# Kernel tuning notes

Hardware: AMD Instinct MI355X
Metric: run time of the kernel (lower is better)

The kernel has to match this reference:

```python
import math
import jax, jax.numpy as jnp
import numpy as np

B, T, C, H = 2, 2048, 1024, 16
D = C // H


def get_slopes(n):
    def pow2_slopes(n):
        start = 2.0 ** (-(2.0 ** (-(math.log2(n) - 3))))
        return [start * (start ** i) for i in range(n)]
    if math.log2(n).is_integer():
        return pow2_slopes(n)
    c = 2 ** math.floor(math.log2(n))
    return pow2_slopes(c) + get_slopes(2 * c)[0::2][: n - c]


def setup_inputs() -> dict:
    key = jax.random.key(0)
    ks = jax.random.split(key, 5)
    std = 0.02
    x = jax.random.normal(ks[0], (B, T, C), dtype=jnp.float32)
    Wq = std * jax.random.normal(ks[1], (C, C), dtype=jnp.float32)
    Wk = std * jax.random.normal(ks[2], (C, C), dtype=jnp.float32)
    Wv = std * jax.random.normal(ks[3], (C, C), dtype=jnp.float32)
    Wo = (std / math.sqrt(24)) * jax.random.normal(ks[4], (C, C), dtype=jnp.float32)
    z = jnp.zeros((C,), dtype=jnp.float32)
    return {"x": x, "Wq": Wq, "bq": z, "Wk": Wk, "bk": z, "Wv": Wv, "bv": z, "Wo": Wo, "bo": z}


def reference(x, Wq, bq, Wk, bk, Wv, bv, Wo, bo):
    b, t, c = x.shape
    h, d = H, c // H
    # qkv projections: nn.Linear computes x @ W.T + b
    q = (x @ Wq.T + bq).reshape(b, t, h, d).transpose(0, 2, 1, 3)  # [B,H,T,D]
    k = (x @ Wk.T + bk).reshape(b, t, h, d).transpose(0, 2, 1, 3)
    v = (x @ Wv.T + bv).reshape(b, t, h, d).transpose(0, 2, 1, 3)

    att = jnp.einsum("bhqd,bhkd->bhqk", q, k) * (1.0 / math.sqrt(d))

    # ALiBi bias: -slope_h * (i - j) on the lower triangle, 0 above
    slopes = jnp.asarray(get_slopes(h), dtype=x.dtype)  # [H]
    i = jnp.arange(t)
    rel = jnp.tril(i[:, None] - i[None, :]).astype(x.dtype)  # [T,T]
    alibi = -slopes[:, None, None] * rel  # [H,T,T]
    att = att + alibi[None, :, :, :]

    causal = jnp.tril(jnp.ones((t, t), dtype=bool))
    att = jnp.where(causal[None, None, :, :], att, -jnp.inf)
    att = jax.nn.softmax(att, axis=-1)

    y = jnp.einsum("bhqk,bhkd->bhqd", att, v)
    y = y.transpose(0, 2, 1, 3).reshape(b, t, c)
    return y @ Wo.T + bo
```

## Files before the change

### kernel.cpp

```cpp
#include <hip/hip_runtime.h>
#include <hip/hip_bf16.h>
#include <cstdint>
#include <cstddef>

#define B_ 2
#define T_ 2048
#define C_ 1024
#define H_ 16
#define D_ 64
#define BT_ (B_*T_)
#define QKV_S 3072

typedef __bf16 bf16;
typedef __bf16 bf16x4 __attribute__((ext_vector_type(4)));
typedef __bf16 bf16x8 __attribute__((ext_vector_type(8)));
typedef float f32x4 __attribute__((ext_vector_type(4)));

__global__ __launch_bounds__(256) void cast_all(const float* __restrict__ x,
                                                const float* __restrict__ wq,
                                                const float* __restrict__ wk,
                                                const float* __restrict__ wv,
                                                const float* __restrict__ wo,
                                                const float* __restrict__ bq,
                                                const float* __restrict__ bk,
                                                const float* __restrict__ bv,
                                                bf16* __restrict__ xb,
                                                bf16* __restrict__ wqkvb,
                                                bf16* __restrict__ wob,
                                                float* __restrict__ bqkv) {
  const int X4 = (BT_ * C_) / 4;
  const int W4 = (C_ * C_) / 4;
  int i = blockIdx.x * blockDim.x + threadIdx.x;
  if (i >= X4 + 4 * W4 + 768) return;
  if (i >= X4 + 4 * W4) {
    int idx = i - (X4 + 4 * W4);
    int w = idx >> 8, off = idx & 255;
    const float* src = (w == 0) ? bq : (w == 1) ? bk : bv;
    reinterpret_cast<float4*>(bqkv + w * C_)[off] = reinterpret_cast<const float4*>(src)[off];
    return;
  }
  const float* src;
  bf16* dst;
  int off;
  if (i < X4) {
    src = x; dst = xb; off = i;
  } else {
    int k = i - X4;
    int w = k >> 18;
    off = k & (W4 - 1);
    src = (w == 0) ? wq : (w == 1) ? wk : (w == 2) ? wv : wo;
    dst = (w < 3) ? (wqkvb + (size_t)w * C_ * C_) : wob;
  }
  float4 v = reinterpret_cast<const float4*>(src)[off];
  bf16x4 o;
  o[0] = (bf16)v.x; o[1] = (bf16)v.y; o[2] = (bf16)v.z; o[3] = (bf16)v.w;
  *reinterpret_cast<bf16x4*>(dst + (size_t)off * 4) = o;
}

template<typename OutT, bool FUSE_VT>
__global__ __launch_bounds__(256) void gemm_bt(const bf16* __restrict__ A,
                                               const bf16* __restrict__ Bm,
                                               const float* __restrict__ bias,
                                               OutT* __restrict__ Cout,
                                               bf16* __restrict__ VtOut,
                                               int M, int N, int K) {
  __shared__ bf16 As[3][128 * 32];
  __shared__ bf16 Bs[3][128 * 32];
  const int tid = threadIdx.x;
  const int wid = tid >> 6, lane = tid & 63;
  const int grp = lane >> 4, li = lane & 15;
  const int wr = wid >> 1, wc = wid & 1;
  const int m0 = blockIdx.y * 128, n0 = blockIdx.x * 128;

  f32x4 acc[4][4] = {};

  const int srow = lane >> 2;
  const int scol = (lane & 3) * 8;

  auto stage = [&](int k0, int bufi) __attribute__((always_inline)) {
#pragma unroll
    for (int p = 0; p < 2; ++p) {
      const int rbase = (p * 4 + wid) * 16;
      const bf16* ga = A + (size_t)(m0 + rbase + srow) * K + (k0 + scol);
      const bf16* gb = Bm + (size_t)(n0 + rbase + srow) * K + (k0 + scol);
      __builtin_amdgcn_global_load_lds((__attribute__((address_space(1))) void*)ga,
                                       (__attribute__((address_space(3))) void*)(&As[bufi][(p * 4 + wid) * 512]), 16, 0, 0);
      __builtin_amdgcn_global_load_lds((__attribute__((address_space(1))) void*)gb,
                                       (__attribute__((address_space(3))) void*)(&Bs[bufi][(p * 4 + wid) * 512]), 16, 0, 0);
    }
  };

  const int nt = K >> 5;
  stage(0, 0);
  if (nt > 1) stage(32, 1);
  int r = 0;
  for (int t = 0; t < nt; ++t) {
    if (t + 1 < nt) asm volatile("s_waitcnt vmcnt(4)\ns_barrier" ::: "memory");
    else            asm volatile("s_waitcnt vmcnt(0)\ns_barrier" ::: "memory");
    if (t + 2 < nt) stage((t + 2) * 32, (r == 0) ? 2 : r - 1);

    bf16x8 af[4], bfr[4];
#pragma unroll
    for (int m = 0; m < 4; ++m)
      af[m] = *reinterpret_cast<const bf16x8*>(&As[r][(wr * 64 + m * 16 + li) * 32 + grp * 8]);
#pragma unroll
    for (int n = 0; n < 4; ++n)
      bfr[n] = *reinterpret_cast<const bf16x8*>(&Bs[r][(wc * 64 + n * 16 + li) * 32 + grp * 8]);
#pragma unroll
    for (int m = 0; m < 4; ++m)
#pragma unroll
      for (int n = 0; n < 4; ++n)
        acc[m][n] = __builtin_amdgcn_mfma_f32_16x16x32_bf16(af[m], bfr[n], acc[m][n], 0, 0, 0);

    r = (r == 2) ? 0 : r + 1;
  }

  float bcol[4];
#pragma unroll
  for (int n = 0; n < 4; ++n) bcol[n] = bias[n0 + wc * 64 + n * 16 + li];

  if (FUSE_VT && n0 >= 2 * C_) {
#pragma unroll
    for (int m = 0; m < 4; ++m) {
      const int row0 = m0 + wr * 64 + m * 16 + grp * 4;
      const int b = row0 >> 11, t = row0 & (T_ - 1);
#pragma unroll
      for (int n = 0; n < 4; ++n) {
        const int hd = (n0 - 2 * C_) + wc * 64 + n * 16 + li;
        bf16x4 o4;
#pragma unroll
        for (int j = 0; j < 4; ++j) o4[j] = (bf16)(acc[m][n][j] + bcol[n]);
        *reinterpret_cast<bf16x4*>(VtOut + ((size_t)(b * C_ + hd)) * T_ + t) = o4;
      }
    }
  } else {
#pragma unroll
    for (int m = 0; m < 4; ++m) {
#pragma unroll
      for (int n = 0; n < 4; ++n) {
        const int col = n0 + wc * 64 + n * 16 + li;
#pragma unroll
        for (int j = 0; j < 4; ++j) {
          const int row = m0 + wr * 64 + m * 16 + grp * 4 + j;
          float v = acc[m][n][j] + bcol[n];
          Cout[(size_t)row * N + col] = (OutT)v;
        }
      }
    }
  }
}

__global__ __launch_bounds__(512) void attn_kernel(const bf16* __restrict__ qkv,
                                                   const bf16* __restrict__ Vt,
                                                   bf16* __restrict__ Y) {
  __shared__ bf16 Ks[4][64 * 64];
  __shared__ bf16 Vs[4][64 * 64];
  __shared__ bf16 Ps[8 * 16 * 72];

  const int tid = threadIdx.x;
  const int wid = tid >> 6, lane = tid & 63;
  const int grp = lane >> 4, li = lane & 15;
  const int bh = blockIdx.y;
  const int b = bh >> 4, h = bh & 15;
  const float slope = exp2f(-0.5f * (float)(h + 1));

  bf16* Pw = Ps + wid * (16 * 72);

  const bf16* Kbase = qkv + (size_t)b * T_ * QKV_S + C_ + (size_t)h * D_;
  const bf16* Vbase = Vt + (size_t)bh * D_ * T_;

  const int strow = tid >> 3;
  const int stswz = ((tid & 7) * 16) ^ ((strow & 7) << 4);
  const int rsw = (li & 7) << 4;

  auto stage = [&](int kv0, int bufi) __attribute__((always_inline)) {
    const bf16* gk = Kbase + (size_t)(kv0 + strow) * QKV_S + (stswz >> 1);
    const bf16* gv = Vbase + (size_t)strow * T_ + kv0 + (stswz >> 1);
    __builtin_amdgcn_global_load_lds((__attribute__((address_space(1))) void*)gk,
                                     (__attribute__((address_space(3))) void*)(&Ks[bufi][wid * 512]), 16, 0, 0);
    __builtin_amdgcn_global_load_lds((__attribute__((address_space(1))) void*)gv,
                                     (__attribute__((address_space(3))) void*)(&Vs[bufi][wid * 512]), 16, 0, 0);
  };

  auto do_qtile = [&](int QT) __attribute__((always_inline)) {
    const int q0 = QT * 128;
    const int wq0 = q0 + wid * 16;
    const int qi = wq0 + li;

    bf16x8 qf[2];
    {
      const bf16* qrow = qkv + (size_t)(b * T_ + qi) * QKV_S + h * D_;
      qf[0] = *reinterpret_cast<const bf16x8*>(qrow + grp * 8);
      qf[1] = *reinterpret_cast<const bf16x8*>(qrow + 32 + grp * 8);
#pragma unroll
      for (int c = 0; c < 2; ++c)
#pragma unroll
        for (int j = 0; j < 8; ++j)
          qf[c][j] = (bf16)((float)qf[c][j] * 0.125f);
    }

    f32x4 oacc[4] = {};
    float mrun = -1e30f, lrun = 0.f;

    auto compute = [&](int kv0, int bufi, bool masked) __attribute__((always_inline)) {
      const char* Kb = (const char*)&Ks[bufi][0];
      const char* Vb = (const char*)&Vs[bufi][0];

      f32x4 s[4] = {};
      __builtin_amdgcn_s_setprio(1);
#pragma unroll
      for (int n = 0; n < 4; ++n) {
        const char* kr = Kb + (n * 16 + li) * 128;
        bf16x8 kf0 = *reinterpret_cast<const bf16x8*>(kr + ((grp * 16) ^ rsw));
        bf16x8 kf1 = *reinterpret_cast<const bf16x8*>(kr + ((64 + grp * 16) ^ rsw));
        s[n] = __builtin_amdgcn_mfma_f32_16x16x32_bf16(kf0, qf[0], s[n], 0, 0, 0);
        s[n] = __builtin_amdgcn_mfma_f32_16x16x32_bf16(kf1, qf[1], s[n], 0, 0, 0);
      }
      __builtin_amdgcn_s_setprio(0);

      bf16x8 vr[2][4];
#pragma unroll
      for (int kc = 0; kc < 2; ++kc)
#pragma unroll
        for (int nd = 0; nd < 4; ++nd) {
          const char* vrp = Vb + (nd * 16 + li) * 128;
          vr[kc][nd] = *reinterpret_cast<const bf16x8*>(vrp + ((kc * 64 + grp * 16) ^ rsw));
        }

      float p[4][4];
      float rm = -1e30f;
#pragma unroll
      for (int n = 0; n < 4; ++n)
#pragma unroll
        for (int j = 0; j < 4; ++j) {
          const int kv = kv0 + n * 16 + grp * 4 + j;
          float sv = fmaf(-slope, (float)(qi - kv), s[n][j]);
          if (masked) sv = (kv <= qi) ? sv : -1e30f;
          p[n][j] = sv;
          rm = fmaxf(rm, sv);
        }
      rm = fmaxf(rm, __shfl_xor(rm, 16, 64));
      rm = fmaxf(rm, __shfl_xor(rm, 32, 64));
      if (!__all(rm - mrun <= 8.0f)) {
        const float mnew = fmaxf(mrun, rm);
        const float alpha = __expf(mrun - mnew);
        mrun = mnew;
        lrun *= alpha;
#pragma unroll
        for (int nd = 0; nd < 4; ++nd)
#pragma unroll
          for (int j = 0; j < 4; ++j)
            oacc[nd][j] *= alpha;
      }
      float rs = 0.f;
#pragma unroll
      for (int n = 0; n < 4; ++n)
#pragma unroll
        for (int j = 0; j < 4; ++j) {
          float e = __expf(p[n][j] - mrun);
          p[n][j] = e;
          rs += e;
        }
      rs += __shfl_xor(rs, 16, 64);
      rs += __shfl_xor(rs, 32, 64);
      lrun += rs;

#pragma unroll
      for (int n = 0; n < 4; ++n) {
        bf16x4 p4;
#pragma unroll
        for (int j = 0; j < 4; ++j) p4[j] = (bf16)p[n][j];
        *reinterpret_cast<bf16x4*>(Pw + li * 72 + n * 16 + grp * 4) = p4;
      }
      asm volatile("s_waitcnt lgkmcnt(0)" ::: "memory");
      __builtin_amdgcn_sched_barrier(0);

      __builtin_amdgcn_s_setprio(1);
#pragma unroll
      for (int kc = 0; kc < 2; ++kc) {
        bf16x8 pb = *reinterpret_cast<const bf16x8*>(Pw + li * 72 + kc * 32 + grp * 8);
#pragma unroll
        for (int nd = 0; nd < 4; ++nd)
          oacc[nd] = __builtin_amdgcn_mfma_f32_16x16x32_bf16(vr[kc][nd], pb, oacc[nd], 0, 0, 0);
      }
      __builtin_amdgcn_s_setprio(0);
    };

    const int nt = 2 * QT + 2;
    stage((nt - 1) * 64, 0);
    stage((nt - 2) * 64, 1);
    int r = 0;
    for (int t = 0; t < nt; ++t) {
      if (t + 1 < nt) asm volatile("s_waitcnt vmcnt(2)\ns_barrier" ::: "memory");
      else            asm volatile("s_waitcnt vmcnt(0)\ns_barrier" ::: "memory");
      if (t + 2 < nt) stage((nt - 3 - t) * 64, (r == 0) ? 2 : r - 1);
      const int kv0 = (nt - 1 - t) * 64;
      if (kv0 <= wq0) compute(kv0, r, kv0 + 64 > wq0);
      r = (r == 2) ? 0 : r + 1;
    }

    const float rinv = 1.f / lrun;
#pragma unroll
    for (int nd = 0; nd < 4; ++nd) {
      bf16x4 o4;
#pragma unroll
      for (int j = 0; j < 4; ++j) o4[j] = (bf16)(oacc[nd][j] * rinv);
      *reinterpret_cast<bf16x4*>(Pw + li * 72 + nd * 16 + grp * 4) = o4;
    }
    asm volatile("s_waitcnt lgkmcnt(0)" ::: "memory");
    __builtin_amdgcn_sched_barrier(0);
    {
      bf16* yrow = Y + (size_t)(b * T_ + qi) * C_ + h * D_;
#pragma unroll
      for (int c = 0; c < 2; ++c) {
        bf16x8 y8 = *reinterpret_cast<const bf16x8*>(Pw + li * 72 + (c * 4 + grp) * 8);
        *reinterpret_cast<bf16x8*>(yrow + (c * 4 + grp) * 8) = y8;
      }
    }
    __syncthreads();
  };

  do_qtile(15 - (int)blockIdx.x);
  do_qtile((int)blockIdx.x);
}

extern "C" void kernel_launch(void* const* d_in, const int* in_sizes, int n_in,
                              void* d_out, int out_size, void* d_ws, size_t ws_size,
                              hipStream_t stream) {
  const float* x  = (const float*)d_in[0];
  const float* Wq = (const float*)d_in[1];
  const float* bq = (const float*)d_in[2];
  const float* Wk = (const float*)d_in[3];
  const float* bk = (const float*)d_in[4];
  const float* Wv = (const float*)d_in[5];
  const float* bv = (const float*)d_in[6];
  const float* Wo = (const float*)d_in[7];
  const float* bo = (const float*)d_in[8];
  float* out = (float*)d_out;

  char* ws = (char*)d_ws;
  bf16* xb    = (bf16*)ws; ws += (size_t)BT_ * C_ * 2;
  bf16* wqkvb = (bf16*)ws; ws += (size_t)3 * C_ * C_ * 2;
  bf16* wob   = (bf16*)ws; ws += (size_t)C_ * C_ * 2;
  bf16* qkvb  = (bf16*)ws; ws += (size_t)BT_ * QKV_S * 2;
  bf16* vtb   = (bf16*)ws; ws += (size_t)B_ * H_ * D_ * T_ * 2;
  float* bqkv = (float*)ws; ws += (size_t)3 * C_ * 4;
  bf16* yb    = xb;

  {
    const int total = (BT_ * C_ + 4 * C_ * C_) / 4 + 768;
    cast_all<<<dim3((total + 255) / 256), dim3(256), 0, stream>>>(
        x, Wq, Wk, Wv, Wo, bq, bk, bv, xb, wqkvb, wob, bqkv);
  }

  gemm_bt<bf16, true><<<dim3(QKV_S / 128, BT_ / 128), dim3(256), 0, stream>>>(
      xb, wqkvb, bqkv, qkvb, vtb, BT_, QKV_S, C_);

  attn_kernel<<<dim3(8, B_ * H_), dim3(512), 0, stream>>>(qkvb, vtb, yb);

  gemm_bt<float, false><<<dim3(C_ / 128, BT_ / 128), dim3(256), 0, stream>>>(
      yb, wob, bo, out, nullptr, BT_, C_, C_);
}
```

Baseline: 208.2 us.

## Split V transpose into separate kernel and shrink attention blocks to 64 queries

The transposed-V write is removed from the QKV GEMM epilogue and done by a standalone LDS-tiled transpose kernel. The attention kernel moves from 512 threads and 128-query tiles to 256 threads and 64-query tiles, with a 3-deep K/V ring instead of 4 and twice as many blocks. The aim is better occupancy and load balance in attention, and removing the strided epilogue stores from the GEMM. The cost is an extra kernel launch and an extra pass over V through memory.

```diff
diff --git a/kernel.cpp b/kernel.cpp
--- a/kernel.cpp
+++ b/kernel.cpp
@@ -57,12 +57,11 @@
   *reinterpret_cast<bf16x4*>(dst + (size_t)off * 4) = o;
 }
 
-template<typename OutT, bool FUSE_VT>
+template<typename OutT>
 __global__ __launch_bounds__(256) void gemm_bt(const bf16* __restrict__ A,
                                                const bf16* __restrict__ Bm,
                                                const float* __restrict__ bias,
                                                OutT* __restrict__ Cout,
-                                               bf16* __restrict__ VtOut,
                                                int M, int N, int K) {
   __shared__ bf16 As[3][128 * 32];
   __shared__ bf16 Bs[3][128 * 32];
@@ -118,44 +117,52 @@
   float bcol[4];
 #pragma unroll
   for (int n = 0; n < 4; ++n) bcol[n] = bias[n0 + wc * 64 + n * 16 + li];
-
-  if (FUSE_VT && n0 >= 2 * C_) {
-#pragma unroll
-    for (int m = 0; m < 4; ++m) {
-      const int row0 = m0 + wr * 64 + m * 16 + grp * 4;
-      const int b = row0 >> 11, t = row0 & (T_ - 1);
-#pragma unroll
-      for (int n = 0; n < 4; ++n) {
-        const int hd = (n0 - 2 * C_) + wc * 64 + n * 16 + li;
-        bf16x4 o4;
-#pragma unroll
-        for (int j = 0; j < 4; ++j) o4[j] = (bf16)(acc[m][n][j] + bcol[n]);
-        *reinterpret_cast<bf16x4*>(VtOut + ((size_t)(b * C_ + hd)) * T_ + t) = o4;
-      }
-    }
-  } else {
-#pragma unroll
-    for (int m = 0; m < 4; ++m) {
-#pragma unroll
-      for (int n = 0; n < 4; ++n) {
-        const int col = n0 + wc * 64 + n * 16 + li;
-#pragma unroll
-        for (int j = 0; j < 4; ++j) {
-          const int row = m0 + wr * 64 + m * 16 + grp * 4 + j;
-          float v = acc[m][n][j] + bcol[n];
-          Cout[(size_t)row * N + col] = (OutT)v;
-        }
-      }
-    }
-  }
-}
-
-__global__ __launch_bounds__(512) void attn_kernel(const bf16* __restrict__ qkv,
+#pragma unroll
+  for (int m = 0; m < 4; ++m) {
+#pragma unroll
+    for (int n = 0; n < 4; ++n) {
+      const int col = n0 + wc * 64 + n * 16 + li;
+#pragma unroll
+      for (int j = 0; j < 4; ++j) {
+        const int row = m0 + wr * 64 + m * 16 + grp * 4 + j;
+        float v = acc[m][n][j] + bcol[n];
+        Cout[(size_t)row * N + col] = (OutT)v;
+      }
+    }
+  }
+}
+
+__global__ __launch_bounds__(256) void transpose_v(const bf16* __restrict__ qkv,
+                                                   bf16* __restrict__ Vt) {
+  __shared__ bf16 tile[64 * 72];
+  const int tid = threadIdx.x;
+  const int t0 = blockIdx.x * 64, bh = blockIdx.y;
+  const int b = bh >> 4, h = bh & 15;
+#pragma unroll
+  for (int p = 0; p < 2; ++p) {
+    int idx = p * 256 + tid;
+    int r = idx >> 3, c = (idx & 7) * 8;
+    bf16x8 v = *reinterpret_cast<const bf16x8*>(qkv + (size_t)(b * T_ + t0 + r) * QKV_S + 2 * C_ + h * D_ + c);
+    *reinterpret_cast<bf16x8*>(&tile[r * 72 + c]) = v;
+  }
+  __syncthreads();
+#pragma unroll
+  for (int p = 0; p < 2; ++p) {
+    int idx = p * 256 + tid;
+    int d = idx >> 3, tc = (idx & 7) * 8;
+    bf16x8 o;
+#pragma unroll
+    for (int j = 0; j < 8; ++j) o[j] = tile[(tc + j) * 72 + d];
+    *reinterpret_cast<bf16x8*>(Vt + ((size_t)bh * D_ + d) * T_ + t0 + tc) = o;
+  }
+}
+
+__global__ __launch_bounds__(256) void attn_kernel(const bf16* __restrict__ qkv,
                                                    const bf16* __restrict__ Vt,
                                                    bf16* __restrict__ Y) {
-  __shared__ bf16 Ks[4][64 * 64];
-  __shared__ bf16 Vs[4][64 * 64];
-  __shared__ bf16 Ps[8 * 16 * 72];
+  __shared__ bf16 Ks[3][64 * 64];
+  __shared__ bf16 Vs[3][64 * 64];
+  __shared__ bf16 Ps[4 * 16 * 72];
 
   const int tid = threadIdx.x;
   const int wid = tid >> 6, lane = tid & 63;
@@ -169,21 +176,27 @@
   const bf16* Kbase = qkv + (size_t)b * T_ * QKV_S + C_ + (size_t)h * D_;
   const bf16* Vbase = Vt + (size_t)bh * D_ * T_;
 
-  const int strow = tid >> 3;
-  const int stswz = ((tid & 7) * 16) ^ ((strow & 7) << 4);
   const int rsw = (li & 7) << 4;
 
+  const int srow = lane >> 3;
+  const int sswz = ((lane & 7) * 16) ^ (srow << 4);
+
   auto stage = [&](int kv0, int bufi) __attribute__((always_inline)) {
-    const bf16* gk = Kbase + (size_t)(kv0 + strow) * QKV_S + (stswz >> 1);
-    const bf16* gv = Vbase + (size_t)strow * T_ + kv0 + (stswz >> 1);
-    __builtin_amdgcn_global_load_lds((__attribute__((address_space(1))) void*)gk,
-                                     (__attribute__((address_space(3))) void*)(&Ks[bufi][wid * 512]), 16, 0, 0);
-    __builtin_amdgcn_global_load_lds((__attribute__((address_space(1))) void*)gv,
-                                     (__attribute__((address_space(3))) void*)(&Vs[bufi][wid * 512]), 16, 0, 0);
+#pragma unroll
+    for (int p = 0; p < 2; ++p) {
+      const int rbase = p * 32 + wid * 8;
+      const int row = rbase + srow;
+      const bf16* gk = Kbase + (size_t)(kv0 + row) * QKV_S + (sswz >> 1);
+      const bf16* gv = Vbase + (size_t)row * T_ + kv0 + (sswz >> 1);
+      __builtin_amdgcn_global_load_lds((__attribute__((address_space(1))) void*)gk,
+                                       (__attribute__((address_space(3))) void*)(&Ks[bufi][rbase * 64]), 16, 0, 0);
+      __builtin_amdgcn_global_load_lds((__attribute__((address_space(1))) void*)gv,
+                                       (__attribute__((address_space(3))) void*)(&Vs[bufi][rbase * 64]), 16, 0, 0);
+    }
   };
 
   auto do_qtile = [&](int QT) __attribute__((always_inline)) {
-    const int q0 = QT * 128;
+    const int q0 = QT * 64;
     const int wq0 = q0 + wid * 16;
     const int qi = wq0 + li;
 
@@ -286,12 +299,12 @@
       __builtin_amdgcn_s_setprio(0);
     };
 
-    const int nt = 2 * QT + 2;
+    const int nt = QT + 1;
     stage((nt - 1) * 64, 0);
-    stage((nt - 2) * 64, 1);
+    if (nt > 1) stage((nt - 2) * 64, 1);
     int r = 0;
     for (int t = 0; t < nt; ++t) {
-      if (t + 1 < nt) asm volatile("s_waitcnt vmcnt(2)\ns_barrier" ::: "memory");
+      if (t + 1 < nt) asm volatile("s_waitcnt vmcnt(4)\ns_barrier" ::: "memory");
       else            asm volatile("s_waitcnt vmcnt(0)\ns_barrier" ::: "memory");
       if (t + 2 < nt) stage((nt - 3 - t) * 64, (r == 0) ? 2 : r - 1);
       const int kv0 = (nt - 1 - t) * 64;
@@ -320,7 +333,7 @@
     __syncthreads();
   };
 
-  do_qtile(15 - (int)blockIdx.x);
+  do_qtile(31 - (int)blockIdx.x);
   do_qtile((int)blockIdx.x);
 }
 
@@ -353,11 +366,13 @@
         x, Wq, Wk, Wv, Wo, bq, bk, bv, xb, wqkvb, wob, bqkv);
   }
 
-  gemm_bt<bf16, true><<<dim3(QKV_S / 128, BT_ / 128), dim3(256), 0, stream>>>(
-      xb, wqkvb, bqkv, qkvb, vtb, BT_, QKV_S, C_);
-
-  attn_kernel<<<dim3(8, B_ * H_), dim3(512), 0, stream>>>(qkvb, vtb, yb);
-
-  gemm_bt<float, false><<<dim3(C_ / 128, BT_ / 128), dim3(256), 0, stream>>>(
-      yb, wob, bo, out, nullptr, BT_, C_, C_);
-}
+  gemm_bt<bf16><<<dim3(QKV_S / 128, BT_ / 128), dim3(256), 0, stream>>>(
+      xb, wqkvb, bqkv, qkvb, BT_, QKV_S, C_);
+
+  transpose_v<<<dim3(T_ / 64, B_ * H_), dim3(256), 0, stream>>>(qkvb, vtb);
+
+  attn_kernel<<<dim3(16, B_ * H_), dim3(256), 0, stream>>>(qkvb, vtb, yb);
+
+  gemm_bt<float><<<dim3(C_ / 128, BT_ / 128), dim3(256), 0, stream>>>(
+      yb, wob, bo, out, BT_, C_, C_);
+}
```

After: 215.3 us. 3.4% more time.
